# Kernel optimization log

Hardware: AMD Instinct MI355X
Metric: run time of the kernel (lower is better)

Reference implementation:

```python
import jax, jax.numpy as jnp
import numpy as np

B, T, HID = 2, 2048, 2048
NH, NKV, HD = 32, 8, 64
SCALE = HD ** -0.5
ROPE_THETA = 10000.0


def _rope_tables(key):
    # standard HF llama rope: cos/sin of shape [B, T, head_dim]
    inv_freq = 1.0 / (ROPE_THETA ** (jnp.arange(0, HD, 2, dtype=jnp.float32) / HD))
    pos = jnp.arange(T, dtype=jnp.float32)
    freqs = pos[:, None] * inv_freq[None, :]            # [T, HD/2]
    emb = jnp.concatenate([freqs, freqs], axis=-1)      # [T, HD]
    cos = jnp.broadcast_to(jnp.cos(emb)[None], (B, T, HD))
    sin = jnp.broadcast_to(jnp.sin(emb)[None], (B, T, HD))
    return cos, sin


def setup_inputs() -> dict:
    key = jax.random.key(0)
    ks = jax.random.split(key, 5)
    hidden_states = jax.random.normal(ks[0], (B, T, HID), dtype=jnp.float32)
    cos, sin = _rope_tables(key)
    s = 0.02
    wq = jax.random.normal(ks[1], (NH * HD, HID), dtype=jnp.float32) * s
    wk = jax.random.normal(ks[2], (NKV * HD, HID), dtype=jnp.float32) * s
    wv = jax.random.normal(ks[3], (NKV * HD, HID), dtype=jnp.float32) * s
    wo = jax.random.normal(ks[4], (HID, NH * HD), dtype=jnp.float32) * s
    return {"hidden_states": hidden_states, "cos": cos, "sin": sin,
            "wq": wq, "wk": wk, "wv": wv, "wo": wo}


def _rotate_half(x):
    x1, x2 = jnp.split(x, 2, axis=-1)
    return jnp.concatenate([-x2, x1], axis=-1)


def _apply_rope(q, k, cos, sin):
    # q: [B, NH, T, HD], k: [B, NKV, T, HD]; cos/sin: [B, T, HD] -> unsqueeze head dim
    c = cos[:, None, :, :]
    s = sin[:, None, :, :]
    q = q * c + _rotate_half(q) * s
    k = k * c + _rotate_half(k) * s
    return q, k


def reference(hidden_states, cos, sin, wq, wk, wv, wo):
    b, t, _ = hidden_states.shape
    # QKV projections (no bias, llama-style)
    q = (hidden_states @ wq.T).reshape(b, t, NH, HD).transpose(0, 2, 1, 3)    # [B,NH,T,HD]
    k = (hidden_states @ wk.T).reshape(b, t, NKV, HD).transpose(0, 2, 1, 3)   # [B,NKV,T,HD]
    v = (hidden_states @ wv.T).reshape(b, t, NKV, HD).transpose(0, 2, 1, 3)
    q, k = _apply_rope(q, k, cos, sin)
    # GQA: repeat kv heads
    rep = NH // NKV
    k = jnp.repeat(k, rep, axis=1)   # [B,NH,T,HD]
    v = jnp.repeat(v, rep, axis=1)
    # causal attention, scaling = head_dim**-0.5
    logits = jnp.einsum("bhqd,bhkd->bhqk", q, k) * SCALE
    causal = jnp.tril(jnp.ones((t, t), dtype=bool))
    logits = jnp.where(causal[None, None], logits, jnp.finfo(logits.dtype).min)
    probs = jax.nn.softmax(logits, axis=-1)
    attn = jnp.einsum("bhqk,bhkd->bhqd", probs, v)       # [B,NH,T,HD]
    attn = attn.transpose(0, 2, 1, 3).reshape(b, t, NH * HD)
    return attn @ wo.T
```

## Files before the change

kernel.cpp:

```cpp
#include <hip/hip_runtime.h>
#include <hip/hip_bf16.h>

#define T_SEQ 2048
#define HID_DIM 2048

typedef __attribute__((ext_vector_type(8))) short short8;
typedef __attribute__((ext_vector_type(4))) short short4v;
typedef __attribute__((ext_vector_type(4))) float f32x4;

#define MFMA16(a, b, c) __builtin_amdgcn_mfma_f32_16x16x32_bf16((a), (b), (c), 0, 0, 0)

static __device__ __forceinline__ ushort f2bf(float f) {
  union { __hip_bfloat16 h; ushort u; } un;
  un.h = __float2bfloat16(f);
  return un.u;
}
static __device__ __forceinline__ float bf2f(ushort u) {
  union { ushort u; __hip_bfloat16 h; } un;
  un.u = u;
  return __bfloat162float(un.h);
}

static __device__ __forceinline__ void gload_lds16(const void* g, void* l) {
  __builtin_amdgcn_global_load_lds(
      (const __attribute__((address_space(1))) void*)g,
      (__attribute__((address_space(3))) void*)l, 16, 0, 0);
}

__global__ __launch_bounds__(256) void cast_kernel(const float* __restrict__ in,
                                                   ushort* __restrict__ out, int n4) {
  int i = blockIdx.x * 256 + threadIdx.x;
  if (i >= n4) return;
  const float4 v = reinterpret_cast<const float4*>(in)[i];
  ushort4 o;
  o.x = f2bf(v.x); o.y = f2bf(v.y); o.z = f2bf(v.z); o.w = f2bf(v.w);
  reinterpret_cast<ushort4*>(out)[i] = o;
}

__device__ __forceinline__ void store_c(float* p, float v) { *p = v; }
__device__ __forceinline__ void store_c(ushort* p, float v) { *p = f2bf(v); }

template <int MODE, typename OutT>
__global__ __launch_bounds__(256) void gemm_bt(const ushort* __restrict__ A,
                                               const ushort* __restrict__ W,
                                               OutT* __restrict__ C,
                                               ushort* __restrict__ vTout,
                                               int M, int N, int K) {
  __shared__ __align__(16) ushort As[128][32];
  __shared__ __align__(16) ushort Bs[128][32];
  const int brow = blockIdx.y * 128, bcol = blockIdx.x * 128;
  const int tid = threadIdx.x;
  const int wid = tid >> 6, lane = tid & 63, l15 = lane & 15, lhi = lane >> 4;
  const int wr = wid >> 1, wc = wid & 1;
  const int srow = tid >> 2, scol = (tid & 3) * 8;

  f32x4 acc[4][4] = {};

  const ushort* a0 = A + (size_t)(brow + srow) * K + scol;
  const ushort* a1 = A + (size_t)(brow + 64 + srow) * K + scol;
  const ushort* w0 = W + (size_t)(bcol + srow) * K + scol;
  const ushort* w1 = W + (size_t)(bcol + 64 + srow) * K + scol;
  ushort* lA0 = &As[0][0] + tid * 8;
  ushort* lA1 = &As[0][0] + 2048 + tid * 8;
  ushort* lB0 = &Bs[0][0] + tid * 8;
  ushort* lB1 = &Bs[0][0] + 2048 + tid * 8;

  for (int k0 = 0; k0 < K; k0 += 32) {
    gload_lds16(a0 + k0, lA0);
    gload_lds16(a1 + k0, lA1);
    gload_lds16(w0 + k0, lB0);
    gload_lds16(w1 + k0, lB1);
    __syncthreads();
    short8 af[4], bfr[4];
#pragma unroll
    for (int m = 0; m < 4; ++m)
      af[m] = *(const short8*)&As[wr * 64 + m * 16 + l15][lhi * 8];
#pragma unroll
    for (int n = 0; n < 4; ++n)
      bfr[n] = *(const short8*)&Bs[wc * 64 + n * 16 + l15][lhi * 8];
#pragma unroll
    for (int m = 0; m < 4; ++m)
#pragma unroll
      for (int n = 0; n < 4; ++n)
        acc[m][n] = MFMA16(af[m], bfr[n], acc[m][n]);
    __syncthreads();
  }

  if (MODE == 2 && bcol >= 2560) {
#pragma unroll
    for (int m = 0; m < 4; ++m) {
      const int row = brow + wr * 64 + m * 16 + lhi * 4;
      const int bb = row >> 11, t = row & 2047;
#pragma unroll
      for (int n = 0; n < 4; ++n) {
        const int cv = bcol + wc * 64 + n * 16 + l15 - 2560;
        const int hk = cv >> 6, dd = cv & 63;
        ushort4 o;
        o.x = f2bf(acc[m][n][0]); o.y = f2bf(acc[m][n][1]);
        o.z = f2bf(acc[m][n][2]); o.w = f2bf(acc[m][n][3]);
        *(ushort4*)&vTout[(size_t)((bb * 8 + hk) * 64 + dd) * 2048 + t] = o;
      }
    }
  } else {
    const int cstride = (MODE == 2) ? 2560 : N;
#pragma unroll
    for (int m = 0; m < 4; ++m) {
      const int row = brow + wr * 64 + m * 16 + lhi * 4;
#pragma unroll
      for (int n = 0; n < 4; ++n) {
        const int col = bcol + wc * 64 + n * 16 + l15;
#pragma unroll
        for (int r = 0; r < 4; ++r)
          store_c(&C[(size_t)(row + r) * cstride + col], acc[m][n][r]);
      }
    }
  }
}

__global__ __launch_bounds__(256) void rope_kernel(ushort* __restrict__ qkv,
                                                   const float* __restrict__ ct,
                                                   const float* __restrict__ st) {
  const int bt = blockIdx.x;
  ushort* row = qkv + (size_t)bt * 2560;
  const float* c = ct + (size_t)bt * 64;
  const float* s = st + (size_t)bt * 64;
  const int tid = threadIdx.x;
#pragma unroll
  for (int it = 0; it < 5; ++it) {
    const int idx = it * 256 + tid;
    const bool isQ = idx < 1024;
    const int sub = isQ ? idx : idx - 1024;
    const int hh = sub >> 5;
    const int p = sub & 31;
    const int col = (isQ ? 0 : 2048) + hh * 64 + p;
    const float x1 = bf2f(row[col]);
    const float x2 = bf2f(row[col + 32]);
    const float cc = c[p], ss = s[p];
    float y1 = x1 * cc - x2 * ss;
    float y2 = x2 * cc + x1 * ss;
    if (isQ) { y1 *= 0.125f; y2 *= 0.125f; }
    row[col] = f2bf(y1);
    row[col + 32] = f2bf(y2);
  }
}

#define PROCESS(SUF, diag_) do {                                              \
    f32x4 s_[4] = {};                                                         \
    __builtin_amdgcn_s_setprio(1);                                            \
    _Pragma("unroll")                                                         \
    for (int n = 0; n < 4; ++n) {                                             \
      const short8 k0_ = *(const short8*)(KtB + n * 2048 + base0);            \
      const short8 k1_ = *(const short8*)(KtB + n * 2048 + base1);            \
      s_[n] = MFMA16(k0_, q##SUF##0, s_[n]);                                  \
      s_[n] = MFMA16(k1_, q##SUF##1, s_[n]);                                  \
    }                                                                         \
    __builtin_amdgcn_s_setprio(0);                                            \
    if (diag_) {                                                              \
      _Pragma("unroll")                                                       \
      for (int n = 0; n < 4; ++n) {                                           \
        const int kb_ = 16 * n + 4 * lhi;                                     \
        _Pragma("unroll")                                                     \
        for (int r = 0; r < 4; ++r)                                           \
          if (kb_ + r > qloc) s_[n][r] = -1e30f;                              \
      }                                                                       \
    }                                                                         \
    float mx_;                                                                \
    {                                                                         \
      const float m0_ = fmaxf(fmaxf(s_[0][0], s_[0][1]), fmaxf(s_[0][2], s_[0][3])); \
      const float m1_ = fmaxf(fmaxf(s_[1][0], s_[1][1]), fmaxf(s_[1][2], s_[1][3])); \
      const float m2_ = fmaxf(fmaxf(s_[2][0], s_[2][1]), fmaxf(s_[2][2], s_[2][3])); \
      const float m3_ = fmaxf(fmaxf(s_[3][0], s_[3][1]), fmaxf(s_[3][2], s_[3][3])); \
      mx_ = fmaxf(fmaxf(m0_, m1_), fmaxf(m2_, m3_));                          \
    }                                                                         \
    mx_ = fmaxf(mx_, __shfl_xor(mx_, 16));                                    \
    mx_ = fmaxf(mx_, __shfl_xor(mx_, 32));                                    \
    const float mn_ = fmaxf(mS##SUF, mx_);                                    \
    const float al_ = __expf(mS##SUF - mn_);                                  \
    _Pragma("unroll")                                                         \
    for (int n = 0; n < 4; ++n) {                                             \
      s_[n][0] = __expf(s_[n][0] - mn_);                                      \
      s_[n][1] = __expf(s_[n][1] - mn_);                                      \
      s_[n][2] = __expf(s_[n][2] - mn_);                                      \
      s_[n][3] = __expf(s_[n][3] - mn_);                                      \
    }                                                                         \
    float rs_;                                                                \
    {                                                                         \
      const float t0_ = (s_[0][0] + s_[0][1]) + (s_[0][2] + s_[0][3]);        \
      const float t1_ = (s_[1][0] + s_[1][1]) + (s_[1][2] + s_[1][3]);        \
      const float t2_ = (s_[2][0] + s_[2][1]) + (s_[2][2] + s_[2][3]);        \
      const float t3_ = (s_[3][0] + s_[3][1]) + (s_[3][2] + s_[3][3]);        \
      rs_ = (t0_ + t1_) + (t2_ + t3_);                                        \
    }                                                                         \
    rs_ += __shfl_xor(rs_, 16);                                               \
    rs_ += __shfl_xor(rs_, 32);                                               \
    lS##SUF = lS##SUF * al_ + rs_;                                            \
    mS##SUF = mn_;                                                            \
    _Pragma("unroll")                                                         \
    for (int n = 0; n < 4; ++n) {                                             \
      short4v pk_;                                                            \
      pk_[0] = (short)f2bf(s_[n][0]);                                         \
      pk_[1] = (short)f2bf(s_[n][1]);                                         \
      pk_[2] = (short)f2bf(s_[n][2]);                                         \
      pk_[3] = (short)f2bf(s_[n][3]);                                         \
      *(short4v*)(PtB + prow + 32 * n + 8 * lhi) = pk_;                       \
    }                                                                         \
    const float al0_ = __shfl(al_, 4 * lhi + 0);                              \
    const float al1_ = __shfl(al_, 4 * lhi + 1);                              \
    const float al2_ = __shfl(al_, 4 * lhi + 2);                              \
    const float al3_ = __shfl(al_, 4 * lhi + 3);                              \
    _Pragma("unroll")                                                         \
    for (int n = 0; n < 4; ++n) {                                             \
      o##SUF[n][0] *= al0_;                                                   \
      o##SUF[n][1] *= al1_;                                                   \
      o##SUF[n][2] *= al2_;                                                   \
      o##SUF[n][3] *= al3_;                                                   \
    }                                                                         \
    {                                                                         \
      const short8 p0_ = *(const short8*)(PtB + prow + 16 * lhi);             \
      const short8 p1_ = *(const short8*)(PtB + prow + 64 + 16 * lhi);        \
      __builtin_amdgcn_s_setprio(1);                                          \
      _Pragma("unroll")                                                       \
      for (int n = 0; n < 4; ++n) {                                           \
        const short8 v0_ = *(const short8*)(VtB + n * 2048 + base0);          \
        const short8 v1_ = *(const short8*)(VtB + n * 2048 + base1);          \
        o##SUF[n] = MFMA16(p0_, v0_, o##SUF[n]);                              \
        o##SUF[n] = MFMA16(p1_, v1_, o##SUF[n]);                              \
      }                                                                       \
      __builtin_amdgcn_s_setprio(0);                                          \
    }                                                                         \
  } while (0)

__global__ __launch_bounds__(256) void attn_kernel(const ushort* __restrict__ qkv,
                                                   const ushort* __restrict__ vT,
                                                   ushort* __restrict__ out) {
  __shared__ __align__(16) ushort Kt[4096];
  __shared__ __align__(16) ushort Vt[4096];
  __shared__ __align__(16) ushort Pt[64 * 72];
  const int bid = blockIdx.x;
  const int j = bid >> 3;
  const int bh = (bid & 7) * 8 + (j & 7);
  const int bx = j >> 3;
  const int b = bh >> 5, h = bh & 31, hkv = h >> 2;
  const int tid = threadIdx.x;
  const int wid = tid >> 6, lane = tid & 63, l15 = lane & 15, lhi = lane >> 4;
  const int qA = bx, qB = 31 - bx;
  const int qloc = wid * 16 + l15;

  short8 qA0, qA1, qB0, qB1;
  {
    const size_t offA = (size_t)(b * T_SEQ + qA * 64 + qloc) * 2560 + h * 64;
    qA0 = *(const short8*)(qkv + offA + lhi * 8);
    qA1 = *(const short8*)(qkv + offA + 32 + lhi * 8);
    const size_t offB = (size_t)(b * T_SEQ + qB * 64 + qloc) * 2560 + h * 64;
    qB0 = *(const short8*)(qkv + offB + lhi * 8);
    qB1 = *(const short8*)(qkv + offB + 32 + lhi * 8);
  }

  f32x4 oA[4] = {}, oB[4] = {};
  float mSA = -1e30f, lSA = 0.f, mSB = -1e30f, lSB = 0.f;

  const int swb = (l15 & 7) << 4;
  const int base0 = l15 * 128 + ((lhi * 16) ^ swb);
  const int base1 = l15 * 128 + ((64 + lhi * 16) ^ swb);
  const char* KtB = (const char*)Kt;
  const char* VtB = (const char*)Vt;
  char* PtB = (char*)Pt;
  const int prow = qloc * 144;

  const int srow = tid >> 3, sgrp = tid & 7;
  const int d0s = ((sgrp ^ (srow & 7)) * 8);
  const ushort* kb_g = qkv + (size_t)b * T_SEQ * 2560 + 2048 + hkv * 64;
  const ushort* vb_g = vT + (size_t)(b * 8 + hkv) * 64 * 2048;
  ushort* ldsK = Kt + tid * 8;
  ushort* ldsV = Vt + tid * 8;

  for (int kt = 0; kt <= qB; ++kt) {
    const int ktb = kt * 64;
    gload_lds16(kb_g + (size_t)(ktb + srow) * 2560 + d0s, ldsK);
    gload_lds16(kb_g + (size_t)(ktb + 32 + srow) * 2560 + d0s, ldsK + 2048);
    gload_lds16(vb_g + (size_t)srow * 2048 + ktb + d0s, ldsV);
    gload_lds16(vb_g + (size_t)(32 + srow) * 2048 + ktb + d0s, ldsV + 2048);
    __syncthreads();
    PROCESS(B, kt == qB);
    if (kt <= qA) PROCESS(A, kt == qA);
    __syncthreads();
  }

  {
    const float invA = 1.f / lSA;
    const float i0 = __shfl(invA, 4 * lhi + 0), i1 = __shfl(invA, 4 * lhi + 1);
    const float i2 = __shfl(invA, 4 * lhi + 2), i3 = __shfl(invA, 4 * lhi + 3);
    const size_t orow = (size_t)(b * T_SEQ + qA * 64 + wid * 16 + lhi * 4);
#pragma unroll
    for (int n = 0; n < 4; ++n) {
      out[(orow + 0) * 2048 + h * 64 + n * 16 + l15] = f2bf(oA[n][0] * i0);
      out[(orow + 1) * 2048 + h * 64 + n * 16 + l15] = f2bf(oA[n][1] * i1);
      out[(orow + 2) * 2048 + h * 64 + n * 16 + l15] = f2bf(oA[n][2] * i2);
      out[(orow + 3) * 2048 + h * 64 + n * 16 + l15] = f2bf(oA[n][3] * i3);
    }
  }
  {
    const float invB = 1.f / lSB;
    const float i0 = __shfl(invB, 4 * lhi + 0), i1 = __shfl(invB, 4 * lhi + 1);
    const float i2 = __shfl(invB, 4 * lhi + 2), i3 = __shfl(invB, 4 * lhi + 3);
    const size_t orow = (size_t)(b * T_SEQ + qB * 64 + wid * 16 + lhi * 4);
#pragma unroll
    for (int n = 0; n < 4; ++n) {
      out[(orow + 0) * 2048 + h * 64 + n * 16 + l15] = f2bf(oB[n][0] * i0);
      out[(orow + 1) * 2048 + h * 64 + n * 16 + l15] = f2bf(oB[n][1] * i1);
      out[(orow + 2) * 2048 + h * 64 + n * 16 + l15] = f2bf(oB[n][2] * i2);
      out[(orow + 3) * 2048 + h * 64 + n * 16 + l15] = f2bf(oB[n][3] * i3);
    }
  }
}

extern "C" void kernel_launch(void* const* d_in, const int* in_sizes, int n_in,
                              void* d_out, int out_size, void* d_ws, size_t ws_size,
                              hipStream_t stream) {
  const float* hs   = (const float*)d_in[0];
  const float* cosb = (const float*)d_in[1];
  const float* sinb = (const float*)d_in[2];
  const float* wq   = (const float*)d_in[3];
  const float* wk   = (const float*)d_in[4];
  const float* wv   = (const float*)d_in[5];
  const float* wo   = (const float*)d_in[6];
  float* out = (float*)d_out;

  char* ws = (char*)d_ws;
  ushort* hsb   = (ushort*)(ws);
  ushort* wqkvb = (ushort*)(ws + 16777216);
  ushort* wob   = (ushort*)(ws + 29360128);
  ushort* qkvQK = (ushort*)(ws + 37748736);
  ushort* vTb   = (ushort*)(ws + 58720256);
  ushort* attno = hsb;

  cast_kernel<<<8192, 256, 0, stream>>>(hs, hsb, 2097152);
  cast_kernel<<<4096, 256, 0, stream>>>(wq, wqkvb, 1048576);
  cast_kernel<<<1024, 256, 0, stream>>>(wk, wqkvb + 4194304, 262144);
  cast_kernel<<<1024, 256, 0, stream>>>(wv, wqkvb + 5242880, 262144);
  cast_kernel<<<4096, 256, 0, stream>>>(wo, wob, 1048576);

  gemm_bt<2, ushort><<<dim3(24, 32), 256, 0, stream>>>(hsb, wqkvb, qkvQK, vTb,
                                                       4096, 3072, 2048);

  rope_kernel<<<4096, 256, 0, stream>>>(qkvQK, cosb, sinb);

  attn_kernel<<<1024, 256, 0, stream>>>(qkvQK, vTb, attno);

  gemm_bt<0, float><<<dim3(16, 32), 256, 0, stream>>>(attno, wob, out, nullptr,
                                                      4096, 2048, 2048);
}
```

Before: 341.8 us.

## Replace GEMM with 512-thread double-buffered swizzled-LDS kernel using larger tiles

Replaces the single-buffered 128x128, K=32 GEMM with a 512-thread kernel that uses 256xBN tiles, K=64 steps and double-buffered LDS. The next tile's global-to-LDS loads are issued before computing the current one, with explicit vmcnt waits. An XOR swizzle on the LDS layout is meant to avoid bank conflicts, and s_setprio is raised around the MFMA bursts. Larger tiles raise reuse and overlap load latency. The cost is more LDS use, fewer blocks (192 and 256) on the GPU, and possible tail imbalance.

```diff
diff --git a/kernel.cpp b/kernel.cpp
--- a/kernel.cpp
+++ b/kernel.cpp
@@ -40,78 +40,126 @@
 __device__ __forceinline__ void store_c(float* p, float v) { *p = v; }
 __device__ __forceinline__ void store_c(ushort* p, float v) { *p = f2bf(v); }
 
-template <int MODE, typename OutT>
-__global__ __launch_bounds__(256) void gemm_bt(const ushort* __restrict__ A,
-                                               const ushort* __restrict__ W,
-                                               OutT* __restrict__ C,
-                                               ushort* __restrict__ vTout,
-                                               int M, int N, int K) {
-  __shared__ __align__(16) ushort As[128][32];
-  __shared__ __align__(16) ushort Bs[128][32];
-  const int brow = blockIdx.y * 128, bcol = blockIdx.x * 128;
+template <int MODE, int BN, typename OutT>
+__global__ __launch_bounds__(512) void gemm8p(const ushort* __restrict__ A,
+                                              const ushort* __restrict__ W,
+                                              OutT* __restrict__ C,
+                                              ushort* __restrict__ vTout,
+                                              int M, int N, int K) {
+  constexpr int LA = 4;
+  constexpr int LB = BN / 64;
+  constexpr int NR = BN / 64;
+  __shared__ __align__(16) ushort As[2][256 * 64];
+  __shared__ __align__(16) ushort Bs[2][BN * 64];
   const int tid = threadIdx.x;
-  const int wid = tid >> 6, lane = tid & 63, l15 = lane & 15, lhi = lane >> 4;
-  const int wr = wid >> 1, wc = wid & 1;
-  const int srow = tid >> 2, scol = (tid & 3) * 8;
-
-  f32x4 acc[4][4] = {};
-
-  const ushort* a0 = A + (size_t)(brow + srow) * K + scol;
-  const ushort* a1 = A + (size_t)(brow + 64 + srow) * K + scol;
-  const ushort* w0 = W + (size_t)(bcol + srow) * K + scol;
-  const ushort* w1 = W + (size_t)(bcol + 64 + srow) * K + scol;
-  ushort* lA0 = &As[0][0] + tid * 8;
-  ushort* lA1 = &As[0][0] + 2048 + tid * 8;
-  ushort* lB0 = &Bs[0][0] + tid * 8;
-  ushort* lB1 = &Bs[0][0] + 2048 + tid * 8;
-
-  for (int k0 = 0; k0 < K; k0 += 32) {
-    gload_lds16(a0 + k0, lA0);
-    gload_lds16(a1 + k0, lA1);
-    gload_lds16(w0 + k0, lB0);
-    gload_lds16(w1 + k0, lB1);
-    __syncthreads();
-    short8 af[4], bfr[4];
-#pragma unroll
-    for (int m = 0; m < 4; ++m)
-      af[m] = *(const short8*)&As[wr * 64 + m * 16 + l15][lhi * 8];
-#pragma unroll
-    for (int n = 0; n < 4; ++n)
-      bfr[n] = *(const short8*)&Bs[wc * 64 + n * 16 + l15][lhi * 8];
-#pragma unroll
-    for (int m = 0; m < 4; ++m)
-#pragma unroll
-      for (int n = 0; n < 4; ++n)
-        acc[m][n] = MFMA16(af[m], bfr[n], acc[m][n]);
-    __syncthreads();
-  }
+  const int lane = tid & 63, l15 = lane & 15, lhi = lane >> 4;
+  const int wid = tid >> 6, wm = wid >> 2, wn = wid & 3;
+  const int brow = blockIdx.y * 256, bcol = blockIdx.x * BN;
+  const int nkt = K >> 6;
+
+  const ushort* asrc[LA]; ushort* adst[LA];
+#pragma unroll
+  for (int j = 0; j < LA; ++j) {
+    const int c = tid + 512 * j, row = c >> 3, k16 = c & 7;
+    asrc[j] = A + (size_t)(brow + row) * K + ((k16 ^ (row & 7)) << 3);
+    adst[j] = &As[0][0] + c * 8;
+  }
+  const ushort* bsrc[LB]; ushort* bdst[LB];
+#pragma unroll
+  for (int j = 0; j < LB; ++j) {
+    const int c = tid + 512 * j, row = c >> 3, k16 = c & 7;
+    bsrc[j] = W + (size_t)(bcol + row) * K + ((k16 ^ (row & 7)) << 3);
+    bdst[j] = &Bs[0][0] + c * 8;
+  }
+
+#define STAGE8(kt_, bf_) do {                                              \
+    _Pragma("unroll")                                                      \
+    for (int j = 0; j < LA; ++j)                                           \
+      gload_lds16(asrc[j] + (kt_) * 64, adst[j] + (bf_) * (256 * 64));     \
+    _Pragma("unroll")                                                      \
+    for (int j = 0; j < LB; ++j)                                           \
+      gload_lds16(bsrc[j] + (kt_) * 64, bdst[j] + (bf_) * (BN * 64));      \
+  } while (0)
+
+  f32x4 acc[8][NR] = {};
+
+  STAGE8(0, 0);
+  for (int kt = 0; kt < nkt; ++kt) {
+    const int bf = kt & 1;
+    if (kt + 1 < nkt) {
+      STAGE8(kt + 1, bf ^ 1);
+      if constexpr (LA + LB == 8) asm volatile("s_waitcnt vmcnt(8)" ::: "memory");
+      else                        asm volatile("s_waitcnt vmcnt(6)" ::: "memory");
+    } else {
+      asm volatile("s_waitcnt vmcnt(0)" ::: "memory");
+    }
+    __builtin_amdgcn_s_barrier();
+    const char* abuf = (const char*)&As[bf][0];
+    const char* bbuf = (const char*)&Bs[bf][0];
+#pragma unroll
+    for (int mh = 0; mh < 2; ++mh) {
+      short8 af[4][2];
+#pragma unroll
+      for (int mi = 0; mi < 4; ++mi) {
+        const int row = wm * 128 + (mh * 4 + mi) * 16 + l15;
+        const int sw = (row & 7) << 4;
+#pragma unroll
+        for (int ks = 0; ks < 2; ++ks)
+          af[mi][ks] = *(const short8*)(abuf + row * 128 + ((ks * 64 + lhi * 16) ^ sw));
+      }
+#pragma unroll
+      for (int nh = 0; nh < NR / 2; ++nh) {
+        short8 bfrag[2][2];
+#pragma unroll
+        for (int ni = 0; ni < 2; ++ni) {
+          const int rowb = wn * (BN / 4) + (nh * 2 + ni) * 16 + l15;
+          const int sw = (rowb & 7) << 4;
+#pragma unroll
+          for (int ks = 0; ks < 2; ++ks)
+            bfrag[ni][ks] = *(const short8*)(bbuf + rowb * 128 + ((ks * 64 + lhi * 16) ^ sw));
+        }
+        __builtin_amdgcn_s_setprio(1);
+#pragma unroll
+        for (int ks = 0; ks < 2; ++ks)
+#pragma unroll
+          for (int mi = 0; mi < 4; ++mi)
+#pragma unroll
+            for (int ni = 0; ni < 2; ++ni)
+              acc[mh * 4 + mi][nh * 2 + ni] =
+                  MFMA16(af[mi][ks], bfrag[ni][ks], acc[mh * 4 + mi][nh * 2 + ni]);
+        __builtin_amdgcn_s_setprio(0);
+      }
+    }
+    __builtin_amdgcn_s_barrier();
+  }
+#undef STAGE8
 
   if (MODE == 2 && bcol >= 2560) {
 #pragma unroll
-    for (int m = 0; m < 4; ++m) {
-      const int row = brow + wr * 64 + m * 16 + lhi * 4;
+    for (int mi8 = 0; mi8 < 8; ++mi8) {
+      const int row = brow + wm * 128 + mi8 * 16 + lhi * 4;
       const int bb = row >> 11, t = row & 2047;
 #pragma unroll
-      for (int n = 0; n < 4; ++n) {
-        const int cv = bcol + wc * 64 + n * 16 + l15 - 2560;
+      for (int ni = 0; ni < NR; ++ni) {
+        const int cv = bcol + wn * (BN / 4) + ni * 16 + l15 - 2560;
         const int hk = cv >> 6, dd = cv & 63;
         ushort4 o;
-        o.x = f2bf(acc[m][n][0]); o.y = f2bf(acc[m][n][1]);
-        o.z = f2bf(acc[m][n][2]); o.w = f2bf(acc[m][n][3]);
+        o.x = f2bf(acc[mi8][ni][0]); o.y = f2bf(acc[mi8][ni][1]);
+        o.z = f2bf(acc[mi8][ni][2]); o.w = f2bf(acc[mi8][ni][3]);
         *(ushort4*)&vTout[(size_t)((bb * 8 + hk) * 64 + dd) * 2048 + t] = o;
       }
     }
   } else {
     const int cstride = (MODE == 2) ? 2560 : N;
 #pragma unroll
-    for (int m = 0; m < 4; ++m) {
-      const int row = brow + wr * 64 + m * 16 + lhi * 4;
-#pragma unroll
-      for (int n = 0; n < 4; ++n) {
-        const int col = bcol + wc * 64 + n * 16 + l15;
+    for (int mi8 = 0; mi8 < 8; ++mi8) {
+      const int row = brow + wm * 128 + mi8 * 16 + lhi * 4;
+#pragma unroll
+      for (int ni = 0; ni < NR; ++ni) {
+        const int col = bcol + wn * (BN / 4) + ni * 16 + l15;
 #pragma unroll
         for (int r = 0; r < 4; ++r)
-          store_c(&C[(size_t)(row + r) * cstride + col], acc[m][n][r]);
+          store_c(&C[(size_t)(row + r) * cstride + col], acc[mi8][ni][r]);
       }
     }
   }
@@ -340,13 +388,13 @@
   cast_kernel<<<1024, 256, 0, stream>>>(wv, wqkvb + 5242880, 262144);
   cast_kernel<<<4096, 256, 0, stream>>>(wo, wob, 1048576);
 
-  gemm_bt<2, ushort><<<dim3(24, 32), 256, 0, stream>>>(hsb, wqkvb, qkvQK, vTb,
-                                                       4096, 3072, 2048);
+  gemm8p<2, 256, ushort><<<dim3(12, 16), 512, 0, stream>>>(hsb, wqkvb, qkvQK,
+                                                           vTb, 4096, 3072, 2048);
 
   rope_kernel<<<4096, 256, 0, stream>>>(qkvQK, cosb, sinb);
 
   attn_kernel<<<1024, 256, 0, stream>>>(qkvQK, vTb, attno);
 
-  gemm_bt<0, float><<<dim3(16, 32), 256, 0, stream>>>(attno, wob, out, nullptr,
-                                                      4096, 2048, 2048);
-}
+  gemm8p<0, 128, float><<<dim3(16, 16), 512, 0, stream>>>(attno, wob, out,
+                                                          nullptr, 4096, 2048, 2048);
+}
```

After: 341.3 us. Within noise of the previous version (-0.2%).
